# Performance work log

Measured on AMD Instinct MI355X. Metric: run time of the kernel, lower is better.

## Reference

```python
import jax, jax.numpy as jnp
import numpy as np

N = 50000       # nodes per side (all node sets share N so concat along dim 1 works)
E = 500000      # edges per relation
B = 64          # graphs for global_mean_pool
C = 32          # per-layer hidden (latent_dim = (32,32) x10)
D = 288         # sum(latent_dim[1:,0]) = 9*32
NUM_CLASSES = 10
NUM_LAYERS = 9


def _tconv(x_s, x_d, ei, Wq, bq, Wk, bk, Wv, bv, Ws, bs, edge_feat=None, We=None):
    """PyG TransformerConv: heads=1, concat=True, beta=False, root_weight=True."""
    q = x_d @ Wq + bq                       # [Nd, C]
    k = x_s @ Wk + bk                       # [Ns, C]
    v = x_s @ Wv + bv                       # [Ns, C]
    src, dst = ei[0], ei[1]
    ke = k[src]                             # gather per edge [E, C]
    ve = v[src]
    if We is not None:                      # lin_edge (bias=False); added to key AND value
        e = edge_feat @ We
        ke = ke + e
        ve = ve + e
    nd = x_d.shape[0]
    logits = jnp.sum(q[dst] * ke, axis=-1) / jnp.sqrt(jnp.float32(C))
    m = jax.ops.segment_max(logits, dst, num_segments=nd)      # segment softmax
    ex = jnp.exp(logits - m[dst])
    denom = jax.ops.segment_sum(ex, dst, num_segments=nd)
    alpha = ex / (denom[dst] + 1e-16)
    agg = jax.ops.segment_sum(ve * alpha[:, None], dst, num_segments=nd)
    return agg + x_d @ Ws + bs              # root/skip linear (lin_skip)


def _forward(inter_emb, edge_attr, uv_target_emb,
             inter_index, uv_target_index, target_uv_index, batch,
             conv_Wq, conv_bq, conv_Wk, conv_bk, conv_Wv, conv_bv,
             conv_Ws, conv_bs, conv_We,
             lin_W1, lin_b1, lin_W2, lin_b2, lin_W3, lin_b3,
             lin_W4, lin_b4, lin_W5, lin_b5, lin_W6, lin_b6):
    f0, f1 = jnp.split(inter_emb, 2, axis=1)            # torch.chunk(x, 2, dim=1)
    edge_feat = jnp.tile(edge_attr[:, None], (1, C))    # at.reshape(-1,1).repeat(1,C)
    states = []
    x = None
    for i in range(NUM_LAYERS):
        p = (conv_Wq[i], conv_bq[i], conv_Wk[i], conv_bk[i],
             conv_Wv[i], conv_bv[i], conv_Ws[i], conv_bs[i])
        if i % 3 == 0:
            xs, xd = (f0, f1) if i == 0 else (x, x)
            x = jnp.tanh(_tconv(xs, xd, inter_index, *p, edge_feat, conv_We[i // 3]))
        elif i % 3 == 1:
            x = jnp.tanh(_tconv(x, uv_target_emb, uv_target_index, *p))
        else:
            x = jnp.tanh(_tconv(uv_target_emb, x, target_uv_index, *p))
        states.append(x)
    h = jnp.concatenate(states, axis=1) @ lin_W1 + lin_b1        # [N, 288]
    sums = jax.ops.segment_sum(h, batch, num_segments=B)
    cnt = jax.ops.segment_sum(jnp.ones((h.shape[0],), h.dtype), batch, num_segments=B)
    pooled = sums / jnp.maximum(cnt, 1.0)[:, None]               # global_mean_pool
    h = jax.nn.relu(pooled @ lin_W2 + lin_b2)
    h = h @ lin_W3 + lin_b3
    h = h @ lin_W4 + lin_b4
    h = h @ lin_W5 + lin_b5
    h = h @ lin_W6 + lin_b6
    return jax.nn.log_softmax(h, axis=-1)                        # [B, NUM_CLASSES]


def setup_inputs():
    key = jax.random.key(0)
    ks = iter(jax.random.split(key, 64))
    def nrm(shape, scale=1.0):
        return jax.random.normal(next(ks), shape, dtype=jnp.float32) * jnp.float32(scale)
    s = 1.0 / np.sqrt(C)
    inp = {
        "inter_emb": nrm((N, 2 * C)),
        "edge_attr": nrm((E,)),
        "uv_target_emb": nrm((N, C)),
        "inter_index": jax.random.randint(next(ks), (2, E), 0, N, dtype=jnp.int32),
        "uv_target_index": jax.random.randint(next(ks), (2, E), 0, N, dtype=jnp.int32),
        "target_uv_index": jax.random.randint(next(ks), (2, E), 0, N, dtype=jnp.int32),
        "batch": jnp.sort(jax.random.randint(next(ks), (N,), 0, B, dtype=jnp.int32)),
        "conv_Wq": nrm((NUM_LAYERS, C, C), s), "conv_bq": nrm((NUM_LAYERS, C), 0.01),
        "conv_Wk": nrm((NUM_LAYERS, C, C), s), "conv_bk": nrm((NUM_LAYERS, C), 0.01),
        "conv_Wv": nrm((NUM_LAYERS, C, C), s), "conv_bv": nrm((NUM_LAYERS, C), 0.01),
        "conv_Ws": nrm((NUM_LAYERS, C, C), s), "conv_bs": nrm((NUM_LAYERS, C), 0.01),
        "conv_We": nrm((3, C, C), s),
        "lin_W1": nrm((D, D), 1.0 / np.sqrt(D)), "lin_b1": nrm((D,), 0.01),
        "lin_W2": nrm((D, D // 2), 1.0 / np.sqrt(D)), "lin_b2": nrm((D // 2,), 0.01),
        "lin_W3": nrm((D // 2, D // 2), 1.0 / np.sqrt(D // 2)), "lin_b3": nrm((D // 2,), 0.01),
        "lin_W4": nrm((D // 2, D // 4), 1.0 / np.sqrt(D // 2)), "lin_b4": nrm((D // 4,), 0.01),
        "lin_W5": nrm((D // 4, D // 4), 1.0 / np.sqrt(D // 4)), "lin_b5": nrm((D // 4,), 0.01),
        "lin_W6": nrm((D // 4, NUM_CLASSES), 1.0 / np.sqrt(D // 4)), "lin_b6": nrm((NUM_CLASSES,), 0.01),
    }
    return inp


def reference(inter_emb, edge_attr, uv_target_emb,
              inter_index, uv_target_index, target_uv_index, batch,
              conv_Wq, conv_bq, conv_Wk, conv_bk, conv_Wv, conv_bv,
              conv_Ws, conv_bs, conv_We,
              lin_W1, lin_b1, lin_W2, lin_b2, lin_W3, lin_b3,
              lin_W4, lin_b4, lin_W5, lin_b5, lin_W6, lin_b6):
    return _forward(inter_emb, edge_attr, uv_target_emb,
                    inter_index, uv_target_index, target_uv_index, batch,
                    conv_Wq, conv_bq, conv_Wk, conv_bk, conv_Wv, conv_bv,
                    conv_Ws, conv_bs, conv_We,
                    lin_W1, lin_b1, lin_W2, lin_b2, lin_W3, lin_b3,
                    lin_W4, lin_b4, lin_W5, lin_b5, lin_W6, lin_b6)
```

## Files before the change

### kernel.cpp

```cpp
#include <hip/hip_runtime.h>
#include <hip/hip_fp16.h>
#include <math.h>

#define RSQRT32 0.17677669529663687f
#define NS 4
#define NC 32
#define MAXBS 12544
#define TILE 2048


__global__ void hist_lds(const int* __restrict__ e0, const int* __restrict__ e1,
                         const int* __restrict__ e2, int E, int N, int BS, int CH,
                         unsigned short* __restrict__ partial) {
    __shared__ unsigned int h[MAXBS];
    int blk = blockIdx.x;
    int c = blk % NC, s = (blk / NC) % NS, r = blk / (NC * NS);
    int lo = s * BS, hi = min(lo + BS, N), nb = hi - lo;
    for (int i = threadIdx.x; i < nb; i += 256) h[i] = 0;
    __syncthreads();
    const int* ei = (r == 0) ? e0 : ((r == 1) ? e1 : e2);
    int ebeg = c * CH, eend = min(ebeg + CH, E);
    const int* dst = ei + E;
    for (int i = ebeg + (int)threadIdx.x; i < eend; i += 256) {
        int d = dst[i];
        if (d >= lo && d < hi) atomicAdd(&h[d - lo], 1u);
    }
    __syncthreads();
    unsigned short* out = partial + ((size_t)blk) * BS;
    for (int i = threadIdx.x; i < nb; i += 256) out[i] = (unsigned short)h[i];
}

__global__ void chunk_scan(unsigned short* __restrict__ partial, int* __restrict__ cnt3,
                           int N, int BS) {
    int t = blockIdx.x * blockDim.x + threadIdx.x;
    int tot = 3 * NS * BS;
    if (t >= tot) return;
    int r = t / (NS * BS);
    int rem = t - r * NS * BS;
    int s = rem / BS, bin = rem - s * BS;
    int d = s * BS + bin;
    if (d >= N) return;
    size_t base = ((size_t)(r * NS + s) * NC) * BS + bin;
    unsigned int run = 0;
    for (int c = 0; c < NC; ++c) {
        unsigned int v = partial[base + (size_t)c * BS];
        partial[base + (size_t)c * BS] = (unsigned short)run;
        run += v;
    }
    cnt3[(size_t)r * N + d] = (int)run;
}

__global__ void scan_tiles_sum(const int* __restrict__ cnt3, int* __restrict__ tsum,
                               int N, int G) {
    int blk = blockIdx.x, r = blk / G, g = blk - r * G;
    int base = g * TILE;
    const int* cnt = cnt3 + (size_t)r * N;
    int s = 0;
    for (int i = threadIdx.x; i < TILE; i += 256) {
        int idx = base + i;
        s += (idx < N) ? cnt[idx] : 0;
    }
    __shared__ int wsum[4];
    for (int m = 32; m; m >>= 1) s += __shfl_down(s, m);
    if ((threadIdx.x & 63) == 0) wsum[threadIdx.x >> 6] = s;
    __syncthreads();
    if (threadIdx.x == 0) tsum[blk] = wsum[0] + wsum[1] + wsum[2] + wsum[3];
}

__global__ void scan_offsets(int* __restrict__ tsum, int* __restrict__ rp3, int N, int G) {
    int r = threadIdx.x;
    if (r < 3) {
        int run = 0;
        for (int g = 0; g < G; ++g) { int v = tsum[r * G + g]; tsum[r * G + g] = run; run += v; }
        rp3[(size_t)r * (N + 1) + N] = run;
    }
}

__global__ void scan_write(const int* __restrict__ cnt3, const int* __restrict__ toff,
                           int* __restrict__ rp3, int N, int G) {
    int blk = blockIdx.x, r = blk / G, g = blk - r * G;
    int base = g * TILE;
    const int* cnt = cnt3 + (size_t)r * N;
    int* rp = rp3 + (size_t)r * (N + 1);
    __shared__ int part[256];
    int t = threadIdx.x;
    int v[8]; int s = 0;
    #pragma unroll
    for (int j = 0; j < 8; ++j) {
        int idx = base + t * 8 + j;
        int x = (idx < N) ? cnt[idx] : 0;
        v[j] = s; s += x;
    }
    part[t] = s;
    __syncthreads();
    for (int off = 1; off < 256; off <<= 1) {
        int x = (t >= off) ? part[t - off] : 0;
        __syncthreads();
        part[t] += x;
        __syncthreads();
    }
    int texcl = part[t] - s + toff[blk];
    #pragma unroll
    for (int j = 0; j < 8; ++j) {
        int idx = base + t * 8 + j;
        if (idx < N) rp[idx] = texcl + v[j];
    }
}

__global__ void scatter_cs(const int* __restrict__ e0, const int* __restrict__ e1,
                           const int* __restrict__ e2, const float* __restrict__ ea,
                           const unsigned short* __restrict__ partial,
                           const int* __restrict__ rp3,
                           int2* __restrict__ adj0, int* __restrict__ adj12,
                           int E, int N, int BS, int CH) {
    __shared__ unsigned int cur[MAXBS];
    int blk = blockIdx.x;
    int s = blk & (NS - 1);
    int rest = blk >> 2;
    int c = rest % NC, r = rest / NC;
    int pblk = c + NC * (s + NS * r);
    int lo = s * BS, hi = min(lo + BS, N), nb = hi - lo;
    const unsigned short* po = partial + ((size_t)pblk) * BS;
    const int* rp = rp3 + (size_t)r * (N + 1);
    for (int i = threadIdx.x; i < nb; i += 256)
        cur[i] = (unsigned int)rp[lo + i] + (unsigned int)po[i];
    __syncthreads();
    const int* ei = (r == 0) ? e0 : ((r == 1) ? e1 : e2);
    const int* srcp = ei;
    const int* dstp = ei + E;
    int ebeg = c * CH, eend = min(ebeg + CH, E);
    if (r == 0) {
        for (int i = ebeg + (int)threadIdx.x; i < eend; i += 256) {
            int d = dstp[i];
            if (d < lo || d >= hi) continue;
            unsigned int pos = atomicAdd(&cur[d - lo], 1u);
            int2 v; v.x = srcp[i]; v.y = __float_as_int(ea[i]);
            adj0[pos] = v;
        }
    } else {
        int* adj = adj12 + (size_t)(r - 1) * E;
        for (int i = ebeg + (int)threadIdx.x; i < eend; i += 256) {
            int d = dstp[i];
            if (d < lo || d >= hi) continue;
            unsigned int pos = atomicAdd(&cur[d - lo], 1u);
            adj[pos] = srcp[i];
        }
    }
}


__global__ void colsum_kernel(const float* __restrict__ We, float* __restrict__ u) {
    int t = threadIdx.x;
    if (t < 96) {
        int w = t >> 5, j = t & 31;
        const float* W = We + w * 1024;
        float s = 0.f;
        #pragma unroll
        for (int kk = 0; kk < 32; ++kk) s += W[kk * 32 + j];
        u[t] = s;
    }
}

__global__ void bounds_kernel(const int* __restrict__ batch, int* __restrict__ bstart,
                              int* __restrict__ bend, int N) {
    int t = blockIdx.x * blockDim.x + threadIdx.x;
    if (t >= N) return;
    int b = batch[t];
    if (t == 0 || batch[t - 1] != b) bstart[b] = t;
    if (t == N - 1 || batch[t + 1] != b) bend[b] = t + 1;
}

__global__ void qkvs_kernel(
    const float* __restrict__ xs, int ssrc,
    const float* __restrict__ xd, int sdst,
    const float* __restrict__ Wq, const float* __restrict__ bq,
    const float* __restrict__ Wk, const float* __restrict__ bk,
    const float* __restrict__ Wv, const float* __restrict__ bv,
    const float* __restrict__ Ws, const float* __restrict__ bs,
    const float* __restrict__ u,
    float* __restrict__ qb, __half2* __restrict__ kv,
    float* __restrict__ sb, float* __restrict__ qdu, int N)
{
    int lane = threadIdx.x & 63;
    int wid  = __builtin_amdgcn_readfirstlane((int)(threadIdx.x >> 6));
    int wpb  = blockDim.x >> 6;
    int gw   = blockIdx.x * wpb + wid;
    int nw   = gridDim.x * wpb;
    int j    = lane & 31;
    bool lower = lane < 32;

    const float* W1 = lower ? Wq : Wk;
    const float* W2 = lower ? Wv : Ws;
    float rw1[32], rw2[32];
    #pragma unroll
    for (int kk = 0; kk < 32; ++kk) {
        rw1[kk] = W1[kk * 32 + j];
        rw2[kk] = W2[kk * 32 + j];
    }
    float bias1 = lower ? bq[j] : bk[j];
    float bias2 = lower ? bv[j] : bs[j];
    float uj = (u != nullptr) ? u[j] : 0.f;

    for (int n = gw; n < N; n += nw) {
        const float* xdr = xd + (size_t)n * sdst;
        const float* xsr = xs + (size_t)n * ssrc;
        float acc1 = bias1, acc2 = bias2;
        #pragma unroll
        for (int kk = 0; kk < 32; ++kk) {
            float xdv = xdr[kk];
            float xsv = xsr[kk];
            float a  = lower ? xdv : xsv;
            float bb = lower ? xsv : xdv;
            acc1 = fmaf(a,  rw1[kk], acc1);
            acc2 = fmaf(bb, rw2[kk], acc2);
        }
        float kk_ = __shfl(acc1, j + 32);
        if (lower) {
            qb[(size_t)n * 32 + j] = acc1;
            kv[(size_t)n * 32 + j] = __floats2half2_rn(kk_, acc2);
        } else {
            sb[(size_t)n * 32 + j] = acc2;
        }
        if (u != nullptr) {
            float pp = lower ? acc1 * uj : 0.f;
            pp += __shfl_xor(pp, 16);
            pp += __shfl_xor(pp, 8);
            pp += __shfl_xor(pp, 4);
            pp += __shfl_xor(pp, 2);
            pp += __shfl_xor(pp, 1);
            if (lane == 0) qdu[n] = pp * RSQRT32;
        }
    }
}

template<int HAS_EA>
__global__ __launch_bounds__(256, 8)
void agg_kernel(const int* __restrict__ rp, const void* __restrict__ adjv,
    const float* __restrict__ qb, const __half2* __restrict__ kv,
    const float* __restrict__ qdu, const float* __restrict__ u,
    const float* __restrict__ skp, float* __restrict__ xout, int N)
{
    int t = threadIdx.x;
    int w = t >> 6, lane = t & 63;
    int cq = lane & 7;
    int o  = lane >> 3;
    int n = blockIdx.x * 4 + w;
    if (n >= N) return;
    float4 qc = ((const float4*)(qb + (size_t)n * 32))[cq];
    float qd = HAS_EA ? qdu[n] : 0.f;
    float4 uc = HAS_EA ? ((const float4*)u)[cq] : make_float4(0.f, 0.f, 0.f, 0.f);
    int beg = rp[n], end = rp[n + 1];
    float den0 = 0.f, den1 = 0.f;
    float4 num0 = make_float4(0.f, 0.f, 0.f, 0.f);
    float4 num1 = make_float4(0.f, 0.f, 0.f, 0.f);
    const int2* adjE = (const int2*)adjv;
    const int*  adjP = (const int*)adjv;
    int i = beg + o;
    for (; i + 8 < end; i += 16) {
        int s0, s1; float ae0 = 0.f, ae1 = 0.f;
        if (HAS_EA) {
            int2 a0 = adjE[i], a1 = adjE[i + 8];
            s0 = a0.x; s1 = a1.x;
            ae0 = __int_as_float(a0.y); ae1 = __int_as_float(a1.y);
        } else { s0 = adjP[i]; s1 = adjP[i + 8]; }
        uint4 p0 = ((const uint4*)(kv + (size_t)s0 * 32))[cq];
        uint4 p1 = ((const uint4*)(kv + (size_t)s1 * 32))[cq];
        float2 a00 = __half22float2(*(const __half2*)&p0.x);
        float2 a01 = __half22float2(*(const __half2*)&p0.y);
        float2 a02 = __half22float2(*(const __half2*)&p0.z);
        float2 a03 = __half22float2(*(const __half2*)&p0.w);
        float2 a10 = __half22float2(*(const __half2*)&p1.x);
        float2 a11 = __half22float2(*(const __half2*)&p1.y);
        float2 a12 = __half22float2(*(const __half2*)&p1.z);
        float2 a13 = __half22float2(*(const __half2*)&p1.w);
        float d0 = fmaf(qc.x, a00.x, fmaf(qc.y, a01.x, fmaf(qc.z, a02.x, qc.w * a03.x)));
        float d1 = fmaf(qc.x, a10.x, fmaf(qc.y, a11.x, fmaf(qc.z, a12.x, qc.w * a13.x)));
        d0 += __shfl_xor(d0, 4);  d1 += __shfl_xor(d1, 4);
        d0 += __shfl_xor(d0, 2);  d1 += __shfl_xor(d1, 2);
        d0 += __shfl_xor(d0, 1);  d1 += __shfl_xor(d1, 1);
        float ex0 = __expf(fmaf(ae0, qd, d0 * RSQRT32));
        float ex1 = __expf(fmaf(ae1, qd, d1 * RSQRT32));
        den0 += ex0;  den1 += ex1;
        num0.x = fmaf(fmaf(ae0, uc.x, a00.y), ex0, num0.x);
        num0.y = fmaf(fmaf(ae0, uc.y, a01.y), ex0, num0.y);
        num0.z = fmaf(fmaf(ae0, uc.z, a02.y), ex0, num0.z);
        num0.w = fmaf(fmaf(ae0, uc.w, a03.y), ex0, num0.w);
        num1.x = fmaf(fmaf(ae1, uc.x, a10.y), ex1, num1.x);
        num1.y = fmaf(fmaf(ae1, uc.y, a11.y), ex1, num1.y);
        num1.z = fmaf(fmaf(ae1, uc.z, a12.y), ex1, num1.z);
        num1.w = fmaf(fmaf(ae1, uc.w, a13.y), ex1, num1.w);
    }
    for (; i < end; i += 8) {
        int s0; float ae0 = 0.f;
        if (HAS_EA) { int2 a0 = adjE[i]; s0 = a0.x; ae0 = __int_as_float(a0.y); }
        else s0 = adjP[i];
        uint4 p0 = ((const uint4*)(kv + (size_t)s0 * 32))[cq];
        float2 a00 = __half22float2(*(const __half2*)&p0.x);
        float2 a01 = __half22float2(*(const __half2*)&p0.y);
        float2 a02 = __half22float2(*(const __half2*)&p0.z);
        float2 a03 = __half22float2(*(const __half2*)&p0.w);
        float d0 = fmaf(qc.x, a00.x, fmaf(qc.y, a01.x, fmaf(qc.z, a02.x, qc.w * a03.x)));
        d0 += __shfl_xor(d0, 4);
        d0 += __shfl_xor(d0, 2);
        d0 += __shfl_xor(d0, 1);
        float ex0 = __expf(fmaf(ae0, qd, d0 * RSQRT32));
        den0 += ex0;
        num0.x = fmaf(fmaf(ae0, uc.x, a00.y), ex0, num0.x);
        num0.y = fmaf(fmaf(ae0, uc.y, a01.y), ex0, num0.y);
        num0.z = fmaf(fmaf(ae0, uc.z, a02.y), ex0, num0.z);
        num0.w = fmaf(fmaf(ae0, uc.w, a03.y), ex0, num0.w);
    }
    float den = den0 + den1;
    float4 num = make_float4(num0.x + num1.x, num0.y + num1.y,
                             num0.z + num1.z, num0.w + num1.w);
    den   += __shfl_xor(den, 8);   den   += __shfl_xor(den, 16);   den   += __shfl_xor(den, 32);
    num.x += __shfl_xor(num.x, 8); num.x += __shfl_xor(num.x, 16); num.x += __shfl_xor(num.x, 32);
    num.y += __shfl_xor(num.y, 8); num.y += __shfl_xor(num.y, 16); num.y += __shfl_xor(num.y, 32);
    num.z += __shfl_xor(num.z, 8); num.z += __shfl_xor(num.z, 16); num.z += __shfl_xor(num.z, 32);
    num.w += __shfl_xor(num.w, 8); num.w += __shfl_xor(num.w, 16); num.w += __shfl_xor(num.w, 32);
    if (o == 0) {
        float inv = 1.f / (den + 1e-16f);
        float4 sk = ((const float4*)(skp + (size_t)n * 32))[cq];
        float4 ov;
        ov.x = tanhf(fmaf(num.x, inv, sk.x));
        ov.y = tanhf(fmaf(num.y, inv, sk.y));
        ov.z = tanhf(fmaf(num.z, inv, sk.z));
        ov.w = tanhf(fmaf(num.w, inv, sk.w));
        ((float4*)(xout + (size_t)n * 32))[cq] = ov;
    }
}

__global__ void pool_kernel(const float* __restrict__ x,
                            const int* __restrict__ bstart, const int* __restrict__ bend,
                            float* __restrict__ poolsum, int layer_off) {
    __shared__ float red[256];
    int b = blockIdx.x >> 3, sub = blockIdx.x & 7;
    int s0 = bstart[b], s1 = bend[b];
    int cnt = s1 - s0;
    int n0 = s0 + (int)((long long)cnt * sub / 8);
    int n1 = s0 + (int)((long long)cnt * (sub + 1) / 8);
    int t = threadIdx.x, col = t & 31, g = t >> 5;
    float acc = 0.f;
    for (int n = n0 + g; n < n1; n += 8)
        acc += x[(size_t)n * 32 + col];
    red[t] = acc;
    __syncthreads();
    if (t < 32) {
        float s = red[t];
        #pragma unroll
        for (int k = 1; k < 8; ++k) s += red[t + 32 * k];
        atomicAdd(&poolsum[(size_t)b * 288 + layer_off + t], s);
    }
}


__device__ __forceinline__ void gemv_step(const float* __restrict__ W, const float* __restrict__ bias,
    const float* sin_, float* sout, int K, int M, int t, bool do_relu) {
    if (t < M) {
        float acc = bias[t];
        for (int kk = 0; kk < K; ++kk) acc = fmaf(sin_[kk], W[kk * M + t], acc);
        sout[t] = do_relu ? fmaxf(acc, 0.f) : acc;
    }
    __syncthreads();
}

__global__ void head_kernel(const float* __restrict__ poolsum,
    const int* __restrict__ bstart, const int* __restrict__ bend,
    const float* __restrict__ W1, const float* __restrict__ b1,
    const float* __restrict__ W2, const float* __restrict__ b2,
    const float* __restrict__ W3, const float* __restrict__ b3,
    const float* __restrict__ W4, const float* __restrict__ b4,
    const float* __restrict__ W5, const float* __restrict__ b5,
    const float* __restrict__ W6, const float* __restrict__ b6,
    float* __restrict__ out)
{
    __shared__ float ha[288], hb[288];
    __shared__ float lse;
    int b = blockIdx.x, t = threadIdx.x;
    float invc = 1.f / fmaxf((float)(bend[b] - bstart[b]), 1.f);
    if (t < 288) ha[t] = poolsum[(size_t)b * 288 + t] * invc;
    __syncthreads();
    gemv_step(W1, b1, ha, hb, 288, 288, t, false);
    gemv_step(W2, b2, hb, ha, 288, 144, t, true);
    gemv_step(W3, b3, ha, hb, 144, 144, t, false);
    gemv_step(W4, b4, hb, ha, 144, 72,  t, false);
    gemv_step(W5, b5, ha, hb, 72,  72,  t, false);
    gemv_step(W6, b6, hb, ha, 72,  10,  t, false);
    if (t == 0) {
        float m = ha[0];
        for (int i = 1; i < 10; ++i) m = fmaxf(m, ha[i]);
        float ssum = 0.f;
        for (int i = 0; i < 10; ++i) ssum += __expf(ha[i] - m);
        lse = m + logf(ssum);
    }
    __syncthreads();
    if (t < 10) out[b * 10 + t] = ha[t] - lse;
}


extern "C" void kernel_launch(void* const* d_in, const int* in_sizes, int n_in,
                              void* d_out, int out_size, void* d_ws, size_t ws_size,
                              hipStream_t stream)
{
    const float* inter_emb = (const float*)d_in[0];
    const float* edge_attr = (const float*)d_in[1];
    const float* uv_emb    = (const float*)d_in[2];
    const int* inter_idx = (const int*)d_in[3];
    const int* uvt_idx   = (const int*)d_in[4];
    const int* tuv_idx   = (const int*)d_in[5];
    const int* batch     = (const int*)d_in[6];
    const float* cWq = (const float*)d_in[7];  const float* cbq = (const float*)d_in[8];
    const float* cWk = (const float*)d_in[9];  const float* cbk = (const float*)d_in[10];
    const float* cWv = (const float*)d_in[11]; const float* cbv = (const float*)d_in[12];
    const float* cWs = (const float*)d_in[13]; const float* cbs = (const float*)d_in[14];
    const float* cWe = (const float*)d_in[15];
    const float* W1 = (const float*)d_in[16]; const float* b1 = (const float*)d_in[17];
    const float* W2 = (const float*)d_in[18]; const float* b2 = (const float*)d_in[19];
    const float* W3 = (const float*)d_in[20]; const float* b3 = (const float*)d_in[21];
    const float* W4 = (const float*)d_in[22]; const float* b4 = (const float*)d_in[23];
    const float* W5 = (const float*)d_in[24]; const float* b5 = (const float*)d_in[25];
    const float* W6 = (const float*)d_in[26]; const float* b6 = (const float*)d_in[27];

    const int N = in_sizes[2] / 32;
    const int E = in_sizes[1];
    const int B = out_size / 10;
    const int G = (N + TILE - 1) / TILE;
    const int BS = (N + NS - 1) / NS;
    const int CH = (E + NC - 1) / NC;

    char* p = (char*)d_ws;
    auto alloc = [&](size_t bytes) { char* r = p; p += (bytes + 255) & ~(size_t)255; return r; };
    float*   qb    = (float*)alloc((size_t)N * 32 * 4);
    __half2* kv    = (__half2*)alloc((size_t)N * 32 * 4);
    float*   sb    = (float*)alloc((size_t)N * 32 * 4);
    float*   qdu   = (float*)alloc((size_t)N * 4);
    float*   xa    = (float*)alloc((size_t)N * 32 * 4);
    float*   xb    = (float*)alloc((size_t)N * 32 * 4);
    float*   ub    = (float*)alloc(96 * 4);
    float*   poolsum = (float*)alloc((size_t)B * 288 * 4);
    int*     bstart = (int*)alloc((size_t)B * 4);
    int*     bend   = (int*)alloc((size_t)B * 4);
    int*     cnt3  = (int*)alloc((size_t)3 * N * 4);
    int*     rp3   = (int*)alloc((size_t)3 * (N + 1) * 4);
    int*     tsum  = (int*)alloc((size_t)3 * G * 4);
    unsigned short* partial = (unsigned short*)alloc((size_t)3 * NS * NC * BS * 2);
    int2*    adj0  = (int2*)alloc((size_t)E * 8);
    int*     adj12 = (int*)alloc((size_t)2 * E * 4);

    hist_lds<<<3 * NS * NC, 256, 0, stream>>>(inter_idx, uvt_idx, tuv_idx, E, N, BS, CH, partial);
    chunk_scan<<<(3 * NS * BS + 255) / 256, 256, 0, stream>>>(partial, cnt3, N, BS);
    scan_tiles_sum<<<3 * G, 256, 0, stream>>>(cnt3, tsum, N, G);
    scan_offsets<<<1, 64, 0, stream>>>(tsum, rp3, N, G);
    scan_write<<<3 * G, 256, 0, stream>>>(cnt3, tsum, rp3, N, G);
    scatter_cs<<<3 * NS * NC, 256, 0, stream>>>(inter_idx, uvt_idx, tuv_idx, edge_attr,
                                                partial, rp3, adj0, adj12, E, N, BS, CH);

    hipMemsetAsync(poolsum, 0, (size_t)B * 288 * 4, stream);
    hipMemsetAsync(bstart, 0, (size_t)B * 4, stream);
    hipMemsetAsync(bend, 0, (size_t)B * 4, stream);
    colsum_kernel<<<1, 128, 0, stream>>>(cWe, ub);
    bounds_kernel<<<(N + 255) / 256, 256, 0, stream>>>(batch, bstart, bend, N);

    float* xcur = nullptr;
    float* xnext = xa;
    for (int i = 0; i < 9; ++i) {
        int r = i % 3;
        const float* xsrc; int ssrc; const float* xdst; int sdst;
        if (i == 0)      { xsrc = inter_emb; ssrc = 64; xdst = inter_emb + 32; sdst = 64; }
        else if (r == 0) { xsrc = xcur; ssrc = 32; xdst = xcur;  sdst = 32; }
        else if (r == 1) { xsrc = xcur; ssrc = 32; xdst = uv_emb; sdst = 32; }
        else             { xsrc = uv_emb; ssrc = 32; xdst = xcur; sdst = 32; }
        const float* ul = (r == 0) ? (ub + (i / 3) * 32) : nullptr;

        qkvs_kernel<<<1024, 256, 0, stream>>>(xsrc, ssrc, xdst, sdst,
            cWq + i * 1024, cbq + i * 32, cWk + i * 1024, cbk + i * 32,
            cWv + i * 1024, cbv + i * 32, cWs + i * 1024, cbs + i * 32,
            ul, qb, kv, sb, qdu, N);
        const int* rpl = rp3 + (size_t)r * (N + 1);
        if (r == 0) {
            agg_kernel<1><<<(N + 3) / 4, 256, 0, stream>>>(
                rpl, adj0, qb, kv, qdu, ul, sb, xnext, N);
        } else {
            agg_kernel<0><<<(N + 3) / 4, 256, 0, stream>>>(
                rpl, adj12 + (size_t)(r - 1) * E, qb, kv, qdu, ul, sb, xnext, N);
        }
        pool_kernel<<<B * 8, 256, 0, stream>>>(xnext, bstart, bend, poolsum, i * 32);
        xcur = xnext;
        xnext = (xnext == xa) ? xb : xa;
    }

    head_kernel<<<B, 320, 0, stream>>>(poolsum, bstart, bend,
        W1, b1, W2, b2, W3, b3, W4, b4, W5, b5, W6, b6, (float*)d_out);
}
```

Measured before the change: 626.6 us.

## Store gathered K/V in FP8 and split CSR build into more node slices

The per-node K/V table gathered per edge is now packed as FP8 (four channels per 32-bit word, separate K and V words), which halves gather traffic compared to half2. The projection kernel packs values with cvt_pk_fp8 after shuffles, and the aggregation kernel unpacks with cvt_pk_f32_fp8. Separately, the CSR histogram and scatter now use 8 node slices with a smaller LDS buffer, which may improve occupancy of those kernels. FP8 gives much lower precision for the attention logits and values, which risks accuracy.

```diff
diff --git a/kernel.cpp b/kernel.cpp
--- a/kernel.cpp
+++ b/kernel.cpp
@@ -3,10 +3,12 @@
 #include <math.h>
 
 #define RSQRT32 0.17677669529663687f
-#define NS 4
+#define NS 8
 #define NC 32
-#define MAXBS 12544
+#define MAXBS 6336
 #define TILE 2048
+
+typedef float fx2 __attribute__((ext_vector_type(2)));
 
 
 __global__ void hist_lds(const int* __restrict__ e0, const int* __restrict__ e1,
@@ -115,8 +117,8 @@
                            int E, int N, int BS, int CH) {
     __shared__ unsigned int cur[MAXBS];
     int blk = blockIdx.x;
-    int s = blk & (NS - 1);
-    int rest = blk >> 2;
+    int s = blk & 7;
+    int rest = blk >> 3;
     int c = rest % NC, r = rest / NC;
     int pblk = c + NC * (s + NS * r);
     int lo = s * BS, hi = min(lo + BS, N), nb = hi - lo;
@@ -178,7 +180,7 @@
     const float* __restrict__ Wv, const float* __restrict__ bv,
     const float* __restrict__ Ws, const float* __restrict__ bs,
     const float* __restrict__ u,
-    float* __restrict__ qb, __half2* __restrict__ kv,
+    float* __restrict__ qb, uint2* __restrict__ kv8,
     float* __restrict__ sb, float* __restrict__ qdu, int N)
 {
     int lane = threadIdx.x & 63;
@@ -215,9 +217,18 @@
             acc2 = fmaf(bb, rw2[kk], acc2);
         }
         float kk_ = __shfl(acc1, j + 32);
+        float k1 = __shfl_down(kk_, 1), v1 = __shfl_down(acc2, 1);
+        float k2 = __shfl_down(kk_, 2), v2 = __shfl_down(acc2, 2);
+        float k3 = __shfl_down(kk_, 3), v3 = __shfl_down(acc2, 3);
         if (lower) {
             qb[(size_t)n * 32 + j] = acc1;
-            kv[(size_t)n * 32 + j] = __floats2half2_rn(kk_, acc2);
+            if ((j & 3) == 0) {
+                int pk = __builtin_amdgcn_cvt_pk_fp8_f32(kk_, k1, 0, false);
+                pk = __builtin_amdgcn_cvt_pk_fp8_f32(k2, k3, pk, true);
+                int pv = __builtin_amdgcn_cvt_pk_fp8_f32(acc2, v1, 0, false);
+                pv = __builtin_amdgcn_cvt_pk_fp8_f32(v2, v3, pv, true);
+                kv8[(size_t)n * 8 + (j >> 2)] = make_uint2((unsigned)pk, (unsigned)pv);
+            }
         } else {
             sb[(size_t)n * 32 + j] = acc2;
         }
@@ -236,7 +247,7 @@
 template<int HAS_EA>
 __global__ __launch_bounds__(256, 8)
 void agg_kernel(const int* __restrict__ rp, const void* __restrict__ adjv,
-    const float* __restrict__ qb, const __half2* __restrict__ kv,
+    const float* __restrict__ qb, const uint2* __restrict__ kv8,
     const float* __restrict__ qdu, const float* __restrict__ u,
     const float* __restrict__ skp, float* __restrict__ xout, int N)
 {
@@ -263,52 +274,52 @@
             s0 = a0.x; s1 = a1.x;
             ae0 = __int_as_float(a0.y); ae1 = __int_as_float(a1.y);
         } else { s0 = adjP[i]; s1 = adjP[i + 8]; }
-        uint4 p0 = ((const uint4*)(kv + (size_t)s0 * 32))[cq];
-        uint4 p1 = ((const uint4*)(kv + (size_t)s1 * 32))[cq];
-        float2 a00 = __half22float2(*(const __half2*)&p0.x);
-        float2 a01 = __half22float2(*(const __half2*)&p0.y);
-        float2 a02 = __half22float2(*(const __half2*)&p0.z);
-        float2 a03 = __half22float2(*(const __half2*)&p0.w);
-        float2 a10 = __half22float2(*(const __half2*)&p1.x);
-        float2 a11 = __half22float2(*(const __half2*)&p1.y);
-        float2 a12 = __half22float2(*(const __half2*)&p1.z);
-        float2 a13 = __half22float2(*(const __half2*)&p1.w);
-        float d0 = fmaf(qc.x, a00.x, fmaf(qc.y, a01.x, fmaf(qc.z, a02.x, qc.w * a03.x)));
-        float d1 = fmaf(qc.x, a10.x, fmaf(qc.y, a11.x, fmaf(qc.z, a12.x, qc.w * a13.x)));
+        uint2 p0 = kv8[(size_t)s0 * 8 + cq];
+        uint2 p1 = kv8[(size_t)s1 * 8 + cq];
+        fx2 k001 = __builtin_amdgcn_cvt_pk_f32_fp8((int)p0.x, false);
+        fx2 k023 = __builtin_amdgcn_cvt_pk_f32_fp8((int)p0.x, true);
+        fx2 w001 = __builtin_amdgcn_cvt_pk_f32_fp8((int)p0.y, false);
+        fx2 w023 = __builtin_amdgcn_cvt_pk_f32_fp8((int)p0.y, true);
+        fx2 k101 = __builtin_amdgcn_cvt_pk_f32_fp8((int)p1.x, false);
+        fx2 k123 = __builtin_amdgcn_cvt_pk_f32_fp8((int)p1.x, true);
+        fx2 w101 = __builtin_amdgcn_cvt_pk_f32_fp8((int)p1.y, false);
+        fx2 w123 = __builtin_amdgcn_cvt_pk_f32_fp8((int)p1.y, true);
+        float d0 = fmaf(qc.x, k001[0], fmaf(qc.y, k001[1], fmaf(qc.z, k023[0], qc.w * k023[1])));
+        float d1 = fmaf(qc.x, k101[0], fmaf(qc.y, k101[1], fmaf(qc.z, k123[0], qc.w * k123[1])));
         d0 += __shfl_xor(d0, 4);  d1 += __shfl_xor(d1, 4);
         d0 += __shfl_xor(d0, 2);  d1 += __shfl_xor(d1, 2);
         d0 += __shfl_xor(d0, 1);  d1 += __shfl_xor(d1, 1);
         float ex0 = __expf(fmaf(ae0, qd, d0 * RSQRT32));
         float ex1 = __expf(fmaf(ae1, qd, d1 * RSQRT32));
         den0 += ex0;  den1 += ex1;
-        num0.x = fmaf(fmaf(ae0, uc.x, a00.y), ex0, num0.x);
-        num0.y = fmaf(fmaf(ae0, uc.y, a01.y), ex0, num0.y);
-        num0.z = fmaf(fmaf(ae0, uc.z, a02.y), ex0, num0.z);
-        num0.w = fmaf(fmaf(ae0, uc.w, a03.y), ex0, num0.w);
-        num1.x = fmaf(fmaf(ae1, uc.x, a10.y), ex1, num1.x);
-        num1.y = fmaf(fmaf(ae1, uc.y, a11.y), ex1, num1.y);
-        num1.z = fmaf(fmaf(ae1, uc.z, a12.y), ex1, num1.z);
-        num1.w = fmaf(fmaf(ae1, uc.w, a13.y), ex1, num1.w);
+        num0.x = fmaf(fmaf(ae0, uc.x, w001[0]), ex0, num0.x);
+        num0.y = fmaf(fmaf(ae0, uc.y, w001[1]), ex0, num0.y);
+        num0.z = fmaf(fmaf(ae0, uc.z, w023[0]), ex0, num0.z);
+        num0.w = fmaf(fmaf(ae0, uc.w, w023[1]), ex0, num0.w);
+        num1.x = fmaf(fmaf(ae1, uc.x, w101[0]), ex1, num1.x);
+        num1.y = fmaf(fmaf(ae1, uc.y, w101[1]), ex1, num1.y);
+        num1.z = fmaf(fmaf(ae1, uc.z, w123[0]), ex1, num1.z);
+        num1.w = fmaf(fmaf(ae1, uc.w, w123[1]), ex1, num1.w);
     }
     for (; i < end; i += 8) {
         int s0; float ae0 = 0.f;
         if (HAS_EA) { int2 a0 = adjE[i]; s0 = a0.x; ae0 = __int_as_float(a0.y); }
         else s0 = adjP[i];
-        uint4 p0 = ((const uint4*)(kv + (size_t)s0 * 32))[cq];
-        float2 a00 = __half22float2(*(const __half2*)&p0.x);
-        float2 a01 = __half22float2(*(const __half2*)&p0.y);
-        float2 a02 = __half22float2(*(const __half2*)&p0.z);
-        float2 a03 = __half22float2(*(const __half2*)&p0.w);
-        float d0 = fmaf(qc.x, a00.x, fmaf(qc.y, a01.x, fmaf(qc.z, a02.x, qc.w * a03.x)));
+        uint2 p0 = kv8[(size_t)s0 * 8 + cq];
+        fx2 k001 = __builtin_amdgcn_cvt_pk_f32_fp8((int)p0.x, false);
+        fx2 k023 = __builtin_amdgcn_cvt_pk_f32_fp8((int)p0.x, true);
+        fx2 w001 = __builtin_amdgcn_cvt_pk_f32_fp8((int)p0.y, false);
+        fx2 w023 = __builtin_amdgcn_cvt_pk_f32_fp8((int)p0.y, true);
+        float d0 = fmaf(qc.x, k001[0], fmaf(qc.y, k001[1], fmaf(qc.z, k023[0], qc.w * k023[1])));
         d0 += __shfl_xor(d0, 4);
         d0 += __shfl_xor(d0, 2);
         d0 += __shfl_xor(d0, 1);
         float ex0 = __expf(fmaf(ae0, qd, d0 * RSQRT32));
         den0 += ex0;
-        num0.x = fmaf(fmaf(ae0, uc.x, a00.y), ex0, num0.x);
-        num0.y = fmaf(fmaf(ae0, uc.y, a01.y), ex0, num0.y);
-        num0.z = fmaf(fmaf(ae0, uc.z, a02.y), ex0, num0.z);
-        num0.w = fmaf(fmaf(ae0, uc.w, a03.y), ex0, num0.w);
+        num0.x = fmaf(fmaf(ae0, uc.x, w001[0]), ex0, num0.x);
+        num0.y = fmaf(fmaf(ae0, uc.y, w001[1]), ex0, num0.y);
+        num0.z = fmaf(fmaf(ae0, uc.z, w023[0]), ex0, num0.z);
+        num0.w = fmaf(fmaf(ae0, uc.w, w023[1]), ex0, num0.w);
     }
     float den = den0 + den1;
     float4 num = make_float4(num0.x + num1.x, num0.y + num1.y,
@@ -431,7 +442,7 @@
     char* p = (char*)d_ws;
     auto alloc = [&](size_t bytes) { char* r = p; p += (bytes + 255) & ~(size_t)255; return r; };
     float*   qb    = (float*)alloc((size_t)N * 32 * 4);
-    __half2* kv    = (__half2*)alloc((size_t)N * 32 * 4);
+    uint2*   kv8   = (uint2*)alloc((size_t)N * 64);
     float*   sb    = (float*)alloc((size_t)N * 32 * 4);
     float*   qdu   = (float*)alloc((size_t)N * 4);
     float*   xa    = (float*)alloc((size_t)N * 32 * 4);
@@ -475,14 +486,14 @@
         qkvs_kernel<<<1024, 256, 0, stream>>>(xsrc, ssrc, xdst, sdst,
             cWq + i * 1024, cbq + i * 32, cWk + i * 1024, cbk + i * 32,
             cWv + i * 1024, cbv + i * 32, cWs + i * 1024, cbs + i * 32,
-            ul, qb, kv, sb, qdu, N);
+            ul, qb, kv8, sb, qdu, N);
         const int* rpl = rp3 + (size_t)r * (N + 1);
         if (r == 0) {
             agg_kernel<1><<<(N + 3) / 4, 256, 0, stream>>>(
-                rpl, adj0, qb, kv, qdu, ul, sb, xnext, N);
+                rpl, adj0, qb, kv8, qdu, ul, sb, xnext, N);
         } else {
             agg_kernel<0><<<(N + 3) / 4, 256, 0, stream>>>(
-                rpl, adj12 + (size_t)(r - 1) * E, qb, kv, qdu, ul, sb, xnext, N);
+                rpl, adj12 + (size_t)(r - 1) * E, qb, kv8, qdu, ul, sb, xnext, N);
         }
         pool_kernel<<<B * 8, 256, 0, stream>>>(xnext, bstart, bend, poolsum, i * 32);
         xcur = xnext;
```

Result: no change. 627.7 us (+0.2%).
